# Optimization experiments

Hardware: AMD Instinct MI355X
Metric: run time of the kernel (lower is better)

Reference implementation:

```python
import jax, jax.numpy as jnp
import numpy as np

R, S, V, F = 4096, 128, 3, 35  # n_rays, n_samples, n_views(=3 fixed by rgb_fc), in_feat_ch+3


def _kaiming(key, fan_out, fan_in):
    return jax.random.normal(key, (fan_out, fan_in), jnp.float32) * jnp.sqrt(2.0 / fan_in)


def setup_inputs() -> dict:
    key = jax.random.key(0)
    ks = jax.random.split(key, 8)
    rgb_feat = jax.random.normal(ks[0], (R, S, V, F), jnp.float32)
    # base_fc: 105 -> 64 -> 32
    bw1, bw2 = _kaiming(ks[1], 64, 105), _kaiming(ks[2], 32, 64)
    # vis_fc: 32 -> 32 -> 32
    vw1, vw2 = _kaiming(ks[3], 32, 32), _kaiming(ks[4], 32, 32)
    # rgb_fc: 96 -> 32 -> 16 -> 3
    rw1, rw2, rw3 = _kaiming(ks[5], 32, 96), _kaiming(ks[6], 16, 32), _kaiming(ks[7], 3, 16)
    z = jnp.zeros
    return {
        "rgb_feat": rgb_feat,
        "bw1": bw1, "bb1": z((64,)), "bw2": bw2, "bb2": z((32,)),
        "vw1": vw1, "vb1": z((32,)), "vw2": vw2, "vb2": z((32,)),
        "rw1": rw1, "rb1": z((32,)), "rw2": rw2, "rb2": z((16,)), "rw3": rw3, "rb3": z((3,)),
    }


def _lin(x, w, b):
    return x @ w.T + b


def reference(rgb_feat, bw1, bb1, bw2, bb2, vw1, vb1, vw2, vb2,
              rw1, rb1, rw2, rb2, rw3, rb3):
    elu = jax.nn.elu
    num_views = rgb_feat.shape[2]
    rgb_in = rgb_feat[..., :3]
    # fused mean/variance over the views axis (dim=2)
    mean = jnp.mean(rgb_feat, axis=2, keepdims=True)          # [R,S,1,F]
    var = jnp.mean((rgb_feat - mean) ** 2, axis=2, keepdims=True)
    globalfeat = jnp.concatenate([mean, var], axis=-1)         # [R,S,1,2F]
    x = jnp.concatenate(
        [jnp.broadcast_to(globalfeat, (rgb_feat.shape[0], rgb_feat.shape[1], num_views, globalfeat.shape[-1])),
         rgb_feat], axis=-1)                                   # [R,S,V,3F]
    x = elu(_lin(elu(_lin(x, bw1, bb1)), bw2, bb2))            # [R,S,V,32]
    x_vis = elu(_lin(elu(_lin(x / num_views, vw1, vb1)), vw2, vb2))
    x = x + x_vis
    h = x.reshape(x.shape[0], x.shape[1], num_views * 32)      # [R,S,96]
    rgb_out = jax.nn.sigmoid(_lin(elu(_lin(elu(_lin(h, rw1, rb1)), rw2, rb2)), rw3, rb3))
    return (rgb_in, rgb_out)
```

## Files before the change

### kernel.cpp

```cpp
#include <hip/hip_runtime.h>
#include <hip/hip_bf16.h>

#define NPTS      524288
#define OUT2_BASE 4718592

using bf16x8 = __attribute__((ext_vector_type(8))) short;
using f32x4  = __attribute__((ext_vector_type(4))) float;


__device__ __forceinline__ ushort f2bf(float f) {
    union { float f; unsigned u; } v; v.f = f;
    unsigned u = v.u;
    unsigned r = u + 0x7fffu + ((u >> 16) & 1u);
    return (ushort)(r >> 16);
}
__device__ __forceinline__ uint pack2(float a, float b) {
    union { __hip_bfloat162 h; uint u; } cv;
    cv.h = __float22bfloat162_rn(make_float2(a, b));
    return cv.u;
}
__device__ __forceinline__ float eluf(float x) {
    return fmaxf(x, 0.f) + __expf(fminf(x, 0.f)) - 1.f;
}
__device__ __forceinline__ float sigm(float x) { return 1.f / (1.f + __expf(-x)); }

__global__ void prep_k(const float* __restrict__ bw1, const float* __restrict__ bw2,
                       const float* __restrict__ vw1, const float* __restrict__ vw2,
                       const float* __restrict__ rw1, const float* __restrict__ rw2,
                       ushort* __restrict__ w)
{
    int i = blockIdx.x * 256 + threadIdx.x;
    if (i < 6144) {
        int n = i / 96, k = i % 96;
        w[i] = f2bf(k < 70 ? bw1[n * 105 + k] : 0.f);
    } else if (i < 10752) {
        int t = i - 6144, n = t / 72, k = t % 72;
        w[i] = f2bf(k < 35 ? bw1[n * 105 + 70 + k] : 0.f);
    } else if (i < 13056) {
        int t = i - 10752, n = t / 72, k = t % 72;
        w[i] = f2bf(k < 64 ? bw2[n * 64 + k] : 0.f);
    } else if (i < 14336) {
        int t = i - 13056, n = t / 40, k = t % 40;
        w[i] = f2bf(k < 32 ? vw1[n * 32 + k] * (1.f / 3.f) : 0.f);
    } else if (i < 15616) {
        int t = i - 14336, n = t / 40, k = t % 40;
        w[i] = f2bf(k < 32 ? vw2[n * 32 + k] : 0.f);
    } else if (i < 18944) {
        int t = i - 15616, n = t / 104, k = t % 104;
        w[i] = f2bf(k < 96 ? rw1[n * 96 + k] : 0.f);
    } else if (i < 19584) {
        int t = i - 18944, n = t / 40, k = t % 40;
        w[i] = f2bf(k < 32 ? rw2[n * 32 + k] : 0.f);
    }
}

__global__ __launch_bounds__(128, 4) void mlp_k(
    const float* __restrict__ feat, const ushort* __restrict__ w,
    const float* __restrict__ bb1, const float* __restrict__ bb2,
    const float* __restrict__ vb1, const float* __restrict__ vb2,
    const float* __restrict__ rb1, const float* __restrict__ rb2,
    const float* __restrict__ rw3, const float* __restrict__ rb3,
    float* __restrict__ out)
{
    __shared__ __align__(16) ushort shA[3456];
    __shared__ __align__(16) ushort shB[1664];
    __shared__ __align__(16) ushort shC[3456];

    const int tid  = threadIdx.x;
    const int wv   = tid >> 6;
    const int lane = tid & 63;
    const int n16  = lane & 15;
    const int quad = lane >> 4;
    const long long pbase = (long long)blockIdx.x * 16;

    const ushort* WG = w;
    const ushort* WF = w + 6144;
    const ushort* W2 = w + 10752;
    const ushort* V1 = w + 13056;
    const ushort* V2 = w + 14336;
    const ushort* R1 = w + 15616;
    const ushort* R2 = w + 18944;

    float bb1v[2];
#pragma unroll
    for (int ntl = 0; ntl < 2; ++ntl) bb1v[ntl] = bb1[(wv * 2 + ntl) * 16 + n16];
    const float bb2v = bb2[wv * 16 + n16];
    const float vb1v = vb1[wv * 16 + n16];
    const float vb2v = vb2[wv * 16 + n16];
    const float rb1v = rb1[wv * 16 + n16];
    const float rb2v = rb2[n16];

    {
        const uint4 z = {0u, 0u, 0u, 0u};
        uint4* zb = (uint4*)shB;
        for (int i = tid; i < 208; i += 128) zb[i] = z;
        uint4* zc = (uint4*)shC;
        for (int i = tid; i < 432; i += 128) zc[i] = z;
        const float4* f4 = (const float4*)(feat + pbase * 105);
        float4* s4 = (float4*)shA;
        for (int i = tid; i < 420; i += 128) s4[i] = f4[i];
    }
    __syncthreads();

    float* sfeat = (float*)shA;

    {
        float* o1 = out + pbase * 9;
        for (int i = tid; i < 144; i += 128) {
            int p = i / 9, r = i - p * 9, v = r / 3, c = r - v * 3;
            o1[i] = sfeat[p * 105 + v * 35 + c];
        }
        ushort* Xg = shB;
        ushort* Xf = shC;
        for (int i = tid; i < 560; i += 128) {
            int p = i / 35, k = i - p * 35;
            float a = sfeat[p * 105 + k];
            float b = sfeat[p * 105 + 35 + k];
            float c = sfeat[p * 105 + 70 + k];
            float m  = (a + b + c) * (1.f / 3.f);
            float da = a - m, db = b - m, dc = c - m;
            float vv = (da * da + db * db + dc * dc) * (1.f / 3.f);
            uint ab = pack2(a, b);
            Xf[p * 72 + k]          = (ushort)ab;
            Xf[(16 + p) * 72 + k]   = (ushort)(ab >> 16);
            Xf[(32 + p) * 72 + k]   = f2bf(c);
            uint mv = pack2(m, vv);
            Xg[p * 96 + k]          = (ushort)mv;
            Xg[p * 96 + 35 + k]     = (ushort)(mv >> 16);
        }
    }
    __syncthreads();

    const f32x4 Z = {0.f, 0.f, 0.f, 0.f};

    f32x4 Cg[2]    = {Z, Z};
    f32x4 Cf[3][2] = {{Z, Z}, {Z, Z}, {Z, Z}};
#pragma unroll
    for (int ks = 0; ks < 3; ++ks) {
        bf16x8 a = *(const bf16x8*)(shB + n16 * 96 + ks * 32 + quad * 8);
#pragma unroll
        for (int ntl = 0; ntl < 2; ++ntl) {
            bf16x8 b = *(const bf16x8*)(WG + ((wv * 2 + ntl) * 16 + n16) * 96 + ks * 32 + quad * 8);
            Cg[ntl] = __builtin_amdgcn_mfma_f32_16x16x32_bf16(a, b, Cg[ntl], 0, 0, 0);
        }
    }
#pragma unroll
    for (int ks = 0; ks < 2; ++ks) {
        bf16x8 a0 = *(const bf16x8*)(shC + (0 * 16 + n16) * 72 + ks * 32 + quad * 8);
        bf16x8 a1 = *(const bf16x8*)(shC + (1 * 16 + n16) * 72 + ks * 32 + quad * 8);
        bf16x8 a2 = *(const bf16x8*)(shC + (2 * 16 + n16) * 72 + ks * 32 + quad * 8);
#pragma unroll
        for (int ntl = 0; ntl < 2; ++ntl) {
            bf16x8 b = *(const bf16x8*)(WF + ((wv * 2 + ntl) * 16 + n16) * 72 + ks * 32 + quad * 8);
            Cf[0][ntl] = __builtin_amdgcn_mfma_f32_16x16x32_bf16(a0, b, Cf[0][ntl], 0, 0, 0);
            Cf[1][ntl] = __builtin_amdgcn_mfma_f32_16x16x32_bf16(a1, b, Cf[1][ntl], 0, 0, 0);
            Cf[2][ntl] = __builtin_amdgcn_mfma_f32_16x16x32_bf16(a2, b, Cf[2][ntl], 0, 0, 0);
        }
    }
#pragma unroll
    for (int mt = 0; mt < 3; ++mt)
#pragma unroll
        for (int ntl = 0; ntl < 2; ++ntl) {
            float e0 = eluf(Cf[mt][ntl][0] + Cg[ntl][0] + bb1v[ntl]);
            float e1 = eluf(Cf[mt][ntl][1] + Cg[ntl][1] + bb1v[ntl]);
            float e2 = eluf(Cf[mt][ntl][2] + Cg[ntl][2] + bb1v[ntl]);
            float e3 = eluf(Cf[mt][ntl][3] + Cg[ntl][3] + bb1v[ntl]);
            int col = (wv * 2 + ntl) * 16 + n16;
            int r0  = (mt * 16 + quad * 4) * 72 + col;
            uint u01 = pack2(e0, e1), u23 = pack2(e2, e3);
            shA[r0]           = (ushort)u01;
            shA[r0 + 72]      = (ushort)(u01 >> 16);
            shA[r0 + 144]     = (ushort)u23;
            shA[r0 + 216]     = (ushort)(u23 >> 16);
        }
    __syncthreads();

    f32x4 C2[3] = {Z, Z, Z};
#pragma unroll
    for (int ks = 0; ks < 2; ++ks) {
        bf16x8 a0 = *(const bf16x8*)(shA + (0 * 16 + n16) * 72 + ks * 32 + quad * 8);
        bf16x8 a1 = *(const bf16x8*)(shA + (1 * 16 + n16) * 72 + ks * 32 + quad * 8);
        bf16x8 a2 = *(const bf16x8*)(shA + (2 * 16 + n16) * 72 + ks * 32 + quad * 8);
        bf16x8 b  = *(const bf16x8*)(W2 + (wv * 16 + n16) * 72 + ks * 32 + quad * 8);
        C2[0] = __builtin_amdgcn_mfma_f32_16x16x32_bf16(a0, b, C2[0], 0, 0, 0);
        C2[1] = __builtin_amdgcn_mfma_f32_16x16x32_bf16(a1, b, C2[1], 0, 0, 0);
        C2[2] = __builtin_amdgcn_mfma_f32_16x16x32_bf16(a2, b, C2[2], 0, 0, 0);
    }
    __syncthreads();
    float h2r[3][4];
#pragma unroll
    for (int mt = 0; mt < 3; ++mt) {
        float e0 = eluf(C2[mt][0] + bb2v);
        float e1 = eluf(C2[mt][1] + bb2v);
        float e2 = eluf(C2[mt][2] + bb2v);
        float e3 = eluf(C2[mt][3] + bb2v);
        h2r[mt][0] = e0; h2r[mt][1] = e1; h2r[mt][2] = e2; h2r[mt][3] = e3;
        int r0 = (mt * 16 + quad * 4) * 72 + wv * 16 + n16;
        uint u01 = pack2(e0, e1), u23 = pack2(e2, e3);
        shC[r0]       = (ushort)u01;
        shC[r0 + 72]  = (ushort)(u01 >> 16);
        shC[r0 + 144] = (ushort)u23;
        shC[r0 + 216] = (ushort)(u23 >> 16);
    }
    __syncthreads();

    f32x4 T1[3] = {Z, Z, Z};
    {
        bf16x8 a0 = *(const bf16x8*)(shC + (0 * 16 + n16) * 72 + quad * 8);
        bf16x8 a1 = *(const bf16x8*)(shC + (1 * 16 + n16) * 72 + quad * 8);
        bf16x8 a2 = *(const bf16x8*)(shC + (2 * 16 + n16) * 72 + quad * 8);
        bf16x8 b  = *(const bf16x8*)(V1 + (wv * 16 + n16) * 40 + quad * 8);
        T1[0] = __builtin_amdgcn_mfma_f32_16x16x32_bf16(a0, b, T1[0], 0, 0, 0);
        T1[1] = __builtin_amdgcn_mfma_f32_16x16x32_bf16(a1, b, T1[1], 0, 0, 0);
        T1[2] = __builtin_amdgcn_mfma_f32_16x16x32_bf16(a2, b, T1[2], 0, 0, 0);
    }
    __syncthreads();
#pragma unroll
    for (int mt = 0; mt < 3; ++mt) {
        float e0 = eluf(T1[mt][0] + vb1v);
        float e1 = eluf(T1[mt][1] + vb1v);
        float e2 = eluf(T1[mt][2] + vb1v);
        float e3 = eluf(T1[mt][3] + vb1v);
        int r0 = (mt * 16 + quad * 4) * 72 + wv * 16 + n16;
        uint u01 = pack2(e0, e1), u23 = pack2(e2, e3);
        shA[r0]       = (ushort)u01;
        shA[r0 + 72]  = (ushort)(u01 >> 16);
        shA[r0 + 144] = (ushort)u23;
        shA[r0 + 216] = (ushort)(u23 >> 16);
    }
    __syncthreads();

    f32x4 T2[3] = {Z, Z, Z};
    {
        bf16x8 a0 = *(const bf16x8*)(shA + (0 * 16 + n16) * 72 + quad * 8);
        bf16x8 a1 = *(const bf16x8*)(shA + (1 * 16 + n16) * 72 + quad * 8);
        bf16x8 a2 = *(const bf16x8*)(shA + (2 * 16 + n16) * 72 + quad * 8);
        bf16x8 b  = *(const bf16x8*)(V2 + (wv * 16 + n16) * 40 + quad * 8);
        T2[0] = __builtin_amdgcn_mfma_f32_16x16x32_bf16(a0, b, T2[0], 0, 0, 0);
        T2[1] = __builtin_amdgcn_mfma_f32_16x16x32_bf16(a1, b, T2[1], 0, 0, 0);
        T2[2] = __builtin_amdgcn_mfma_f32_16x16x32_bf16(a2, b, T2[2], 0, 0, 0);
    }
    __syncthreads();
#pragma unroll
    for (int mt = 0; mt < 3; ++mt) {
        float x0 = h2r[mt][0] + eluf(T2[mt][0] + vb2v);
        float x1 = h2r[mt][1] + eluf(T2[mt][1] + vb2v);
        float x2v = h2r[mt][2] + eluf(T2[mt][2] + vb2v);
        float x3 = h2r[mt][3] + eluf(T2[mt][3] + vb2v);
        int col = mt * 32 + wv * 16 + n16;
        int r0  = (quad * 4) * 104 + col;
        uint u01 = pack2(x0, x1), u23 = pack2(x2v, x3);
        shB[r0]       = (ushort)u01;
        shB[r0 + 104] = (ushort)(u01 >> 16);
        shB[r0 + 208] = (ushort)u23;
        shB[r0 + 312] = (ushort)(u23 >> 16);
    }
    __syncthreads();

    f32x4 CR = Z;
#pragma unroll
    for (int ks = 0; ks < 3; ++ks) {
        bf16x8 a = *(const bf16x8*)(shB + n16 * 104 + ks * 32 + quad * 8);
        bf16x8 b = *(const bf16x8*)(R1 + (wv * 16 + n16) * 104 + ks * 32 + quad * 8);
        CR = __builtin_amdgcn_mfma_f32_16x16x32_bf16(a, b, CR, 0, 0, 0);
    }
    __syncthreads();
    {
        float e0 = eluf(CR[0] + rb1v);
        float e1 = eluf(CR[1] + rb1v);
        float e2 = eluf(CR[2] + rb1v);
        float e3 = eluf(CR[3] + rb1v);
        int r0 = (quad * 4) * 40 + wv * 16 + n16;
        uint u01 = pack2(e0, e1), u23 = pack2(e2, e3);
        shC[r0]       = (ushort)u01;
        shC[r0 + 40]  = (ushort)(u01 >> 16);
        shC[r0 + 80]  = (ushort)u23;
        shC[r0 + 120] = (ushort)(u23 >> 16);
    }
    __syncthreads();

    f32x4 C3 = Z;
    {
        bf16x8 a = *(const bf16x8*)(shC + n16 * 40 + quad * 8);
        bf16x8 b = *(const bf16x8*)(R2 + n16 * 40 + quad * 8);
        C3 = __builtin_amdgcn_mfma_f32_16x16x32_bf16(a, b, C3, 0, 0, 0);
    }
    __syncthreads();
    {
        float* r2b = (float*)shA;
#pragma unroll
        for (int rr = 0; rr < 2; ++rr) {
            int r = 2 * wv + rr;
            r2b[(quad * 4 + r) * 20 + n16] = eluf(C3[r] + rb2v);
        }
    }
    __syncthreads();

    if (tid < 48) {
        const float* r2b = (const float*)shA;
        int p = tid / 3, c = tid - p * 3;
        float s = rb3[c];
        const float* rr = r2b + p * 20;
        const float* w3 = rw3 + c * 16;
#pragma unroll
        for (int k2 = 0; k2 < 16; ++k2) s += rr[k2] * w3[k2];
        out[OUT2_BASE + pbase * 3 + tid] = sigm(s);
    }
}

extern "C" void kernel_launch(void* const* d_in, const int* in_sizes, int n_in,
                              void* d_out, int out_size, void* d_ws, size_t ws_size,
                              hipStream_t stream) {
    const float* feat = (const float*)d_in[0];
    const float* bw1  = (const float*)d_in[1];
    const float* bb1  = (const float*)d_in[2];
    const float* bw2  = (const float*)d_in[3];
    const float* bb2  = (const float*)d_in[4];
    const float* vw1  = (const float*)d_in[5];
    const float* vb1  = (const float*)d_in[6];
    const float* vw2  = (const float*)d_in[7];
    const float* vb2  = (const float*)d_in[8];
    const float* rw1  = (const float*)d_in[9];
    const float* rb1  = (const float*)d_in[10];
    const float* rw2  = (const float*)d_in[11];
    const float* rb2  = (const float*)d_in[12];
    const float* rw3  = (const float*)d_in[13];
    const float* rb3  = (const float*)d_in[14];
    ushort* w  = (ushort*)d_ws;
    float* out = (float*)d_out;

    hipLaunchKernelGGL(prep_k, dim3(77), dim3(256), 0, stream,
                       bw1, bw2, vw1, vw2, rw1, rw2, w);
    hipLaunchKernelGGL(mlp_k, dim3(NPTS / 16), dim3(128), 0, stream,
                       feat, w, bb1, bb2, vb1, vb2, rb1, rb2, rw3, rb3, out);
}
```

Baseline: 434.6 us.

## Load features straight from global into padded bf16 tiles, drop extra barriers

The kernel no longer stages the fp32 feature block in shared memory. Each thread now loads 8-float chunks straight from global memory, computes mean and variance, and writes packed bf16 rows with 16-byte stores. The base weight layout is re-padded so mean and variance sit at aligned offsets, only the pad columns are zeroed, and five barriers after MFMA accumulation are removed. The final dot product is vectorised with float4 loads. The changes aim to cut LDS traffic, scalar stores and sync stalls, but they rely on careful buffer reuse ordering and an edge case for the last row read.

```diff
diff --git a/kernel.cpp b/kernel.cpp
--- a/kernel.cpp
+++ b/kernel.cpp
@@ -23,6 +23,11 @@
     return fmaxf(x, 0.f) + __expf(fminf(x, 0.f)) - 1.f;
 }
 __device__ __forceinline__ float sigm(float x) { return 1.f / (1.f + __expf(-x)); }
+
+__device__ __forceinline__ void load8(const float* __restrict__ p, float* d) {
+    __builtin_memcpy(d, p, 16);
+    __builtin_memcpy(d + 4, p + 4, 16);
+}
 
 __global__ void prep_k(const float* __restrict__ bw1, const float* __restrict__ bw2,
                        const float* __restrict__ vw1, const float* __restrict__ vw2,
@@ -32,7 +37,10 @@
     int i = blockIdx.x * 256 + threadIdx.x;
     if (i < 6144) {
         int n = i / 96, k = i % 96;
-        w[i] = f2bf(k < 70 ? bw1[n * 105 + k] : 0.f);
+        float val = 0.f;
+        if (k < 35)                 val = bw1[n * 105 + k];
+        else if (k >= 40 && k < 75) val = bw1[n * 105 + 35 + (k - 40)];
+        w[i] = f2bf(val);
     } else if (i < 10752) {
         int t = i - 6144, n = t / 72, k = t % 72;
         w[i] = f2bf(k < 35 ? bw1[n * 105 + 70 + k] : 0.f);
@@ -91,42 +99,59 @@
     const float rb2v = rb2[n16];
 
     {
-        const uint4 z = {0u, 0u, 0u, 0u};
-        uint4* zb = (uint4*)shB;
-        for (int i = tid; i < 208; i += 128) zb[i] = z;
+        const uint4 z = make_uint4(0u, 0u, 0u, 0u);
         uint4* zc = (uint4*)shC;
-        for (int i = tid; i < 432; i += 128) zc[i] = z;
-        const float4* f4 = (const float4*)(feat + pbase * 105);
-        float4* s4 = (float4*)shA;
-        for (int i = tid; i < 420; i += 128) s4[i] = f4[i];
-    }
-    __syncthreads();
-
-    float* sfeat = (float*)shA;
-
-    {
-        float* o1 = out + pbase * 9;
+        for (int i = tid; i < 144; i += 128) {
+            int r = i / 3, c = i - r * 3;
+            zc[r * 9 + 5 + c] = z;
+        }
+        if (tid < 32) {
+            uint4* zb = (uint4*)shB;
+            int r = tid >> 1, c = tid & 1;
+            zb[r * 12 + 10 + c] = z;
+        }
         for (int i = tid; i < 144; i += 128) {
             int p = i / 9, r = i - p * 9, v = r / 3, c = r - v * 3;
-            o1[i] = sfeat[p * 105 + v * 35 + c];
-        }
-        ushort* Xg = shB;
-        ushort* Xf = shC;
-        for (int i = tid; i < 560; i += 128) {
-            int p = i / 35, k = i - p * 35;
-            float a = sfeat[p * 105 + k];
-            float b = sfeat[p * 105 + 35 + k];
-            float c = sfeat[p * 105 + 70 + k];
-            float m  = (a + b + c) * (1.f / 3.f);
-            float da = a - m, db = b - m, dc = c - m;
-            float vv = (da * da + db * db + dc * dc) * (1.f / 3.f);
-            uint ab = pack2(a, b);
-            Xf[p * 72 + k]          = (ushort)ab;
-            Xf[(16 + p) * 72 + k]   = (ushort)(ab >> 16);
-            Xf[(32 + p) * 72 + k]   = f2bf(c);
-            uint mv = pack2(m, vv);
-            Xg[p * 96 + k]          = (ushort)mv;
-            Xg[p * 96 + 35 + k]     = (ushort)(mv >> 16);
+            out[pbase * 9 + i] = feat[(pbase + p) * 105 + v * 35 + c];
+        }
+        if (tid < 80) {
+            int p  = tid / 5;
+            int g  = tid - p * 5;
+            int k8 = g * 8;
+            const float* row = feat + (pbase + p) * 105;
+            float X0[8], X1[8], X2[8];
+            load8(row + k8,      X0);
+            load8(row + 35 + k8, X1);
+            if (k8 == 32 && (pbase + p) == (long long)NPTS - 1) {
+                X2[0] = row[102]; X2[1] = row[103]; X2[2] = row[104];
+                X2[3] = 0.f; X2[4] = 0.f; X2[5] = 0.f; X2[6] = 0.f; X2[7] = 0.f;
+            } else {
+                load8(row + 70 + k8, X2);
+            }
+            float M[8], VV[8];
+#pragma unroll
+            for (int j = 0; j < 8; ++j) {
+                float a = X0[j], b = X1[j], c = X2[j];
+                float m  = (a + b + c) * (1.f / 3.f);
+                float da = a - m, db = b - m, dc = c - m;
+                M[j]  = m;
+                VV[j] = (da * da + db * db + dc * dc) * (1.f / 3.f);
+            }
+            *(uint4*)(shC + p * 72 + k8) =
+                make_uint4(pack2(X0[0], X0[1]), pack2(X0[2], X0[3]),
+                           pack2(X0[4], X0[5]), pack2(X0[6], X0[7]));
+            *(uint4*)(shC + (16 + p) * 72 + k8) =
+                make_uint4(pack2(X1[0], X1[1]), pack2(X1[2], X1[3]),
+                           pack2(X1[4], X1[5]), pack2(X1[6], X1[7]));
+            *(uint4*)(shC + (32 + p) * 72 + k8) =
+                make_uint4(pack2(X2[0], X2[1]), pack2(X2[2], X2[3]),
+                           pack2(X2[4], X2[5]), pack2(X2[6], X2[7]));
+            *(uint4*)(shB + p * 96 + k8) =
+                make_uint4(pack2(M[0], M[1]), pack2(M[2], M[3]),
+                           pack2(M[4], M[5]), pack2(M[6], M[7]));
+            *(uint4*)(shB + p * 96 + 40 + k8) =
+                make_uint4(pack2(VV[0], VV[1]), pack2(VV[2], VV[3]),
+                           pack2(VV[4], VV[5]), pack2(VV[6], VV[7]));
         }
     }
     __syncthreads();
@@ -186,7 +211,6 @@
         C2[1] = __builtin_amdgcn_mfma_f32_16x16x32_bf16(a1, b, C2[1], 0, 0, 0);
         C2[2] = __builtin_amdgcn_mfma_f32_16x16x32_bf16(a2, b, C2[2], 0, 0, 0);
     }
-    __syncthreads();
     float h2r[3][4];
 #pragma unroll
     for (int mt = 0; mt < 3; ++mt) {
@@ -214,7 +238,6 @@
         T1[1] = __builtin_amdgcn_mfma_f32_16x16x32_bf16(a1, b, T1[1], 0, 0, 0);
         T1[2] = __builtin_amdgcn_mfma_f32_16x16x32_bf16(a2, b, T1[2], 0, 0, 0);
     }
-    __syncthreads();
 #pragma unroll
     for (int mt = 0; mt < 3; ++mt) {
         float e0 = eluf(T1[mt][0] + vb1v);
@@ -240,13 +263,12 @@
         T2[1] = __builtin_amdgcn_mfma_f32_16x16x32_bf16(a1, b, T2[1], 0, 0, 0);
         T2[2] = __builtin_amdgcn_mfma_f32_16x16x32_bf16(a2, b, T2[2], 0, 0, 0);
     }
-    __syncthreads();
 #pragma unroll
     for (int mt = 0; mt < 3; ++mt) {
-        float x0 = h2r[mt][0] + eluf(T2[mt][0] + vb2v);
-        float x1 = h2r[mt][1] + eluf(T2[mt][1] + vb2v);
+        float x0  = h2r[mt][0] + eluf(T2[mt][0] + vb2v);
+        float x1  = h2r[mt][1] + eluf(T2[mt][1] + vb2v);
         float x2v = h2r[mt][2] + eluf(T2[mt][2] + vb2v);
-        float x3 = h2r[mt][3] + eluf(T2[mt][3] + vb2v);
+        float x3  = h2r[mt][3] + eluf(T2[mt][3] + vb2v);
         int col = mt * 32 + wv * 16 + n16;
         int r0  = (quad * 4) * 104 + col;
         uint u01 = pack2(x0, x1), u23 = pack2(x2v, x3);
@@ -264,7 +286,6 @@
         bf16x8 b = *(const bf16x8*)(R1 + (wv * 16 + n16) * 104 + ks * 32 + quad * 8);
         CR = __builtin_amdgcn_mfma_f32_16x16x32_bf16(a, b, CR, 0, 0, 0);
     }
-    __syncthreads();
     {
         float e0 = eluf(CR[0] + rb1v);
         float e1 = eluf(CR[1] + rb1v);
@@ -285,7 +306,6 @@
         bf16x8 b = *(const bf16x8*)(R2 + n16 * 40 + quad * 8);
         C3 = __builtin_amdgcn_mfma_f32_16x16x32_bf16(a, b, C3, 0, 0, 0);
     }
-    __syncthreads();
     {
         float* r2b = (float*)shA;
 #pragma unroll
@@ -299,11 +319,15 @@
     if (tid < 48) {
         const float* r2b = (const float*)shA;
         int p = tid / 3, c = tid - p * 3;
+        const float4* rr = (const float4*)(r2b + p * 20);
+        const float4* w3 = (const float4*)(rw3 + c * 16);
+        float4 a0 = rr[0], a1 = rr[1], a2 = rr[2], a3 = rr[3];
+        float4 q0 = w3[0], q1 = w3[1], q2 = w3[2], q3 = w3[3];
         float s = rb3[c];
-        const float* rr = r2b + p * 20;
-        const float* w3 = rw3 + c * 16;
-#pragma unroll
-        for (int k2 = 0; k2 < 16; ++k2) s += rr[k2] * w3[k2];
+        s += a0.x * q0.x + a0.y * q0.y + a0.z * q0.z + a0.w * q0.w;
+        s += a1.x * q1.x + a1.y * q1.y + a1.z * q1.z + a1.w * q1.w;
+        s += a2.x * q2.x + a2.y * q2.y + a2.z * q2.z + a2.w * q2.w;
+        s += a3.x * q3.x + a3.y * q3.y + a3.z * q3.z + a3.w * q3.w;
         out[OUT2_BASE + pbase * 3 + tid] = sigm(s);
     }
 }
```

After: 429.0 us. Within noise of the previous version (-1.3%).
